# Optimization experiments

Measured on AMD Instinct MI355X. Metric: run time of the kernel, lower is better.

The kernel has to match this reference:

```python
import jax, jax.numpy as jnp
import numpy as np

N_INST = 131072      # total patches across all bags
D_EMB = 512          # VGG16 pooling='max' output dim
ATT_UNITS = 128
CLS_UNITS = 512
NUM_BAGS = 256


def setup_inputs() -> dict:
    key = jax.random.key(0)
    ks = jax.random.split(key, 16)
    first_emb = jax.random.normal(ks[0], (N_INST, D_EMB), dtype=jnp.float32)
    first_lab = jnp.sort(jax.random.randint(ks[1], (N_INST,), 0, NUM_BAGS)).astype(jnp.int64)
    s = 0.02
    return {
        "first_emb": first_emb,
        "first_lab": first_lab,
        # first-level attention head: Dense(tanh) -> Dense(1, sigmoid)
        "W_a1": jax.random.normal(ks[2], (D_EMB, ATT_UNITS), dtype=jnp.float32) * s,
        "b_a1": jnp.zeros((ATT_UNITS,), dtype=jnp.float32),
        "w_o1": jax.random.normal(ks[3], (ATT_UNITS, 1), dtype=jnp.float32) * s,
        "b_o1": jnp.zeros((1,), dtype=jnp.float32),
        # second-level attention head
        "W_a2": jax.random.normal(ks[4], (D_EMB, ATT_UNITS), dtype=jnp.float32) * s,
        "b_a2": jnp.zeros((ATT_UNITS,), dtype=jnp.float32),
        "w_o2": jax.random.normal(ks[5], (ATT_UNITS, 1), dtype=jnp.float32) * s,
        "b_o2": jnp.zeros((1,), dtype=jnp.float32),
        # classifier: Dense(CLS_UNITS, linear) -> Dense(1, sigmoid)
        "W_c": jax.random.normal(ks[6], (D_EMB, CLS_UNITS), dtype=jnp.float32) * s,
        "b_c": jnp.zeros((CLS_UNITS,), dtype=jnp.float32),
        "w_out": jax.random.normal(ks[7], (CLS_UNITS, 1), dtype=jnp.float32) * s,
        "b_out": jnp.zeros((1,), dtype=jnp.float32),
    }


def reference(first_emb, first_lab, W_a1, b_a1, w_o1, b_o1,
              W_a2, b_a2, w_o2, b_o2, W_c, b_c, w_out, b_out):
    # --- first-level (instance) attention ---
    a1 = jnp.tanh(first_emb @ W_a1 + b_a1)                 # [N, A]
    att1 = jax.nn.sigmoid(a1 @ w_o1 + b_o1)                # [N, 1]
    # tf: transpose(softmax(transpose(att))) == softmax over the N axis (global)
    fst_att = jax.nn.softmax(att1, axis=0)                 # [N, 1]
    # --- per-bag attention-weighted sum (fused segment reduce) ---
    # replaces the python loop of gather_nd + matmul over contiguous bags
    second_emb = jax.ops.segment_sum(fst_att * first_emb, first_lab,
                                     num_segments=NUM_BAGS)  # [B, D]
    # --- second-level (bag) attention ---
    a2 = jnp.tanh(second_emb @ W_a2 + b_a2)                # [B, A]
    att2 = jax.nn.sigmoid(a2 @ w_o2 + b_o2)                # [B, 1]
    snd_att = jax.nn.softmax(att2.T, axis=-1)              # [1, B]
    outer_bag_emb = snd_att @ second_emb                   # [1, D]
    # --- classifier (dropout is identity at inference) ---
    h = outer_bag_emb @ W_c + b_c                          # [1, CLS]
    pred = jax.nn.sigmoid(h @ w_out + b_out)               # [1, 1]
    return pred
```

## Files before the change

### kernel.cpp

```cpp
#include <hip/hip_runtime.h>
#include <cstdint>
#include <cstddef>

#define N_INST 131072
#define D_EMB  512
#define ATT    128
#define NBAGS  256
#define TILE_I 32
#define LDA    520
#define NBLK   512
#define NTILES (N_INST / TILE_I)
#define TPB    (NTILES / NBLK)

typedef __attribute__((ext_vector_type(8))) short  bf16x8;
typedef __attribute__((ext_vector_type(4))) float  f32x4;
typedef __attribute__((ext_vector_type(4))) unsigned short u16x4;


__device__ inline unsigned short f2b(float f) {
    unsigned u = __builtin_bit_cast(unsigned, f);
    u += 0x7FFFu + ((u >> 16) & 1u);
    return (unsigned short)(u >> 16);
}

__device__ inline float fast_tanh(float x) {
    float e = __expf(2.f * x);
    return 1.f - 2.f / (e + 1.f);
}

__global__ __launch_bounds__(256) void k_prep_wt(
    const float* __restrict__ Wa1, unsigned short* __restrict__ Wt)
{
    const int n = blockIdx.x;
    for (int k = threadIdx.x; k < D_EMB; k += 256)
        Wt[(size_t)n * D_EMB + k] = f2b(Wa1[(size_t)k * ATT + n]);
}

__global__ __launch_bounds__(256, 2) void k_att1(
    const float* __restrict__ emb, const int* __restrict__ lab,
    const unsigned short* __restrict__ Wt, const float* __restrict__ ba1,
    const float* __restrict__ wo1, const float* __restrict__ bo1,
    float* __restrict__ rawr, int R, float* __restrict__ Z1)
{
    __shared__ unsigned short Ash[2][TILE_I * LDA];
    __shared__ float att4[4][TILE_I];
    __shared__ float sval[TILE_I];
    __shared__ int   labs[2][TILE_I];

    const int t  = threadIdx.x;
    const int w  = t >> 6;
    const int l  = t & 63;
    const int l4 = l & 15;
    const int h4 = l >> 4;
    const int n0 = 16 * (2 * w) + l4;
    const int n1 = 16 * (2 * w + 1) + l4;
    float* __restrict__ raw = rawr + (size_t)(blockIdx.x % R) * (NBAGS * D_EMB);

    const float ba1v0 = ba1[n0], ba1v1 = ba1[n1];
    const float wo1v0 = wo1[n0], wo1v1 = wo1[n1];
    float z1acc = 0.f;

    {
        const size_t i0 = (size_t)blockIdx.x * TILE_I;
        float4 v[16];
        #pragma unroll
        for (int j = 0; j < 16; ++j) {
            int idx = j * 256 + t;
            int row = idx >> 7;
            int c4  = (idx & 127) * 4;
            v[j] = *reinterpret_cast<const float4*>(&emb[(i0 + row) * D_EMB + c4]);
        }
        if (t < TILE_I) labs[0][t] = lab[i0 + t];
        #pragma unroll
        for (int j = 0; j < 16; ++j) {
            int idx = j * 256 + t;
            int row = idx >> 7;
            int c4  = (idx & 127) * 4;
            u16x4 b = { f2b(v[j].x), f2b(v[j].y), f2b(v[j].z), f2b(v[j].w) };
            *reinterpret_cast<u16x4*>(&Ash[0][row * LDA + c4]) = b;
        }
    }
    __syncthreads();

    int p = 0;
    for (int it = 0; it < TPB; ++it) {
        const bool hasNext = (it + 1 < TPB);
        const size_t i0n = ((size_t)blockIdx.x + (size_t)(it + 1) * NBLK) * TILE_I;

        float4 v[16];
        int nlab = 0;
        if (hasNext) {
            #pragma unroll
            for (int j = 0; j < 16; ++j) {
                int idx = j * 256 + t;
                int row = idx >> 7;
                int c4  = (idx & 127) * 4;
                v[j] = *reinterpret_cast<const float4*>(
                    &emb[(i0n + row) * D_EMB + c4]);
            }
            if (t < TILE_I) nlab = lab[i0n + t];
        }

        f32x4 acc00 = {0.f,0.f,0.f,0.f}, acc01 = {0.f,0.f,0.f,0.f};
        f32x4 acc10 = {0.f,0.f,0.f,0.f}, acc11 = {0.f,0.f,0.f,0.f};
        #pragma unroll
        for (int ks = 0; ks < 16; ++ks) {
            bf16x8 b0 = *reinterpret_cast<const bf16x8*>(
                &Wt[(size_t)n0 * D_EMB + 32 * ks + 8 * h4]);
            bf16x8 b1 = *reinterpret_cast<const bf16x8*>(
                &Wt[(size_t)n1 * D_EMB + 32 * ks + 8 * h4]);
            bf16x8 a0 = *reinterpret_cast<const bf16x8*>(
                &Ash[p][(l4) * LDA + 32 * ks + 8 * h4]);
            bf16x8 a1 = *reinterpret_cast<const bf16x8*>(
                &Ash[p][(16 + l4) * LDA + 32 * ks + 8 * h4]);
            acc00 = __builtin_amdgcn_mfma_f32_16x16x32_bf16(a0, b0, acc00, 0, 0, 0);
            acc01 = __builtin_amdgcn_mfma_f32_16x16x32_bf16(a0, b1, acc01, 0, 0, 0);
            acc10 = __builtin_amdgcn_mfma_f32_16x16x32_bf16(a1, b0, acc10, 0, 0, 0);
            acc11 = __builtin_amdgcn_mfma_f32_16x16x32_bf16(a1, b1, acc11, 0, 0, 0);
        }

        #pragma unroll
        for (int rt = 0; rt < 2; ++rt) {
            #pragma unroll
            for (int reg = 0; reg < 4; ++reg) {
                float pp = fast_tanh((rt ? acc10[reg] : acc00[reg]) + ba1v0) * wo1v0
                         + fast_tanh((rt ? acc11[reg] : acc01[reg]) + ba1v1) * wo1v1;
                pp += __shfl_xor(pp, 1);
                pp += __shfl_xor(pp, 2);
                pp += __shfl_xor(pp, 4);
                pp += __shfl_xor(pp, 8);
                if (l4 == 0) att4[w][16 * rt + 4 * h4 + reg] = pp;
            }
        }
        __syncthreads();
        if (t < TILE_I) {
            float a  = att4[0][t] + att4[1][t] + att4[2][t] + att4[3][t] + bo1[0];
            float sg = 1.f / (1.f + __expf(-a));
            sval[t]  = __expf(sg);
        }
        __syncthreads();
        if (t < TILE_I) {
            float z = sval[t];
            z += __shfl_xor(z, 1);
            z += __shfl_xor(z, 2);
            z += __shfl_xor(z, 4);
            z += __shfl_xor(z, 8);
            z += __shfl_xor(z, 16);
            if (t == 0) z1acc += z;
        }

        int s0 = 0;
        while (s0 < TILE_I) {
            int bag = labs[p][s0];
            int s1 = s0 + 1;
            while (s1 < TILE_I && labs[p][s1] == bag) ++s1;
            float a0 = 0.f, a1 = 0.f;
            for (int ii = s0; ii < s1; ++ii) {
                unsigned u = *reinterpret_cast<const unsigned*>(
                    &Ash[p][(size_t)ii * LDA + 2 * t]);
                float lo = __builtin_bit_cast(float, u << 16);
                float hi = __builtin_bit_cast(float, u & 0xffff0000u);
                float s  = sval[ii];
                a0 = fmaf(s, lo, a0);
                a1 = fmaf(s, hi, a1);
            }
            atomicAdd(&raw[bag * D_EMB + 2 * t], a0);
            atomicAdd(&raw[bag * D_EMB + 2 * t + 1], a1);
            s0 = s1;
        }
        __syncthreads();

        if (hasNext) {
            #pragma unroll
            for (int j = 0; j < 16; ++j) {
                int idx = j * 256 + t;
                int row = idx >> 7;
                int c4  = (idx & 127) * 4;
                u16x4 b = { f2b(v[j].x), f2b(v[j].y), f2b(v[j].z), f2b(v[j].w) };
                *reinterpret_cast<u16x4*>(&Ash[p ^ 1][row * LDA + c4]) = b;
            }
            if (t < TILE_I) labs[p ^ 1][t] = nlab;
        }
        __syncthreads();
        p ^= 1;
    }
    if (t == 0) atomicAdd(Z1, z1acc);
}

__global__ __launch_bounds__(128) void k_att2(
    const float* __restrict__ Wa2, const float* __restrict__ ba2,
    const float* __restrict__ wo2, const float* __restrict__ bo2,
    float* __restrict__ rawr, int R, const float* __restrict__ Z1,
    float* __restrict__ e2, float* __restrict__ Z2)
{
    __shared__ float sec[D_EMB];
    __shared__ float hh[2];
    const int b = blockIdx.x;
    const int t = threadIdx.x;
    const float zinv = 1.f / Z1[0];
    for (int d = t; d < D_EMB; d += 128) {
        float s = 0.f;
        for (int r = 0; r < R; ++r)
            s += rawr[(size_t)r * (NBAGS * D_EMB) + b * D_EMB + d];
        float v = s * zinv;
        rawr[b * D_EMB + d] = v;
        sec[d] = v;
    }
    __syncthreads();
    float dot = 0.f;
    #pragma unroll 8
    for (int d = 0; d < D_EMB; ++d) dot = fmaf(sec[d], Wa2[d * ATT + t], dot);
    float h = fast_tanh(dot + ba2[t]) * wo2[t];
    #pragma unroll
    for (int m = 1; m < 64; m <<= 1) h += __shfl_xor(h, m);
    if ((t & 63) == 0) hh[t >> 6] = h;
    __syncthreads();
    if (t == 0) {
        float a  = hh[0] + hh[1] + bo2[0];
        float sg = 1.f / (1.f + __expf(-a));
        float e  = __expf(sg);
        e2[b] = e;
        atomicAdd(Z2, e);
    }
}

__global__ __launch_bounds__(256) void k_v(
    const float* __restrict__ Wc, const float* __restrict__ wout,
    float* __restrict__ v)
{
    const int t   = threadIdx.x;
    const int row = blockIdx.x * 8 + (t >> 5);
    const int l   = t & 31;
    float s = 0.f;
    #pragma unroll 4
    for (int c = l; c < 512; c += 32) s = fmaf(Wc[(size_t)row * 512 + c], wout[c], s);
    #pragma unroll
    for (int m = 1; m < 32; m <<= 1) s += __shfl_xor(s, m);
    if (l == 0) v[row] = s;
}

__global__ __launch_bounds__(256) void k_pool(
    const float* __restrict__ raw, const float* __restrict__ e2,
    float* __restrict__ outer)
{
    const int t  = threadIdx.x;
    const int b0 = blockIdx.x * 32;
    float o0 = 0.f, o1 = 0.f;
    for (int b = b0; b < b0 + 32; ++b) {
        float wgt = e2[b];
        float2 r = *reinterpret_cast<const float2*>(&raw[b * D_EMB + 2 * t]);
        o0 = fmaf(wgt, r.x, o0);
        o1 = fmaf(wgt, r.y, o1);
    }
    atomicAdd(&outer[2 * t], o0);
    atomicAdd(&outer[2 * t + 1], o1);
}

__global__ __launch_bounds__(256) void k_cls(
    const float* __restrict__ outer, const float* __restrict__ Z2,
    const float* __restrict__ v, const float* __restrict__ bc,
    const float* __restrict__ wout, const float* __restrict__ bout,
    float* __restrict__ out)
{
    __shared__ float pp[4];
    const int t = threadIdx.x;
    const float z2inv = 1.f / Z2[0];
    float p = (outer[2 * t] * v[2 * t] + outer[2 * t + 1] * v[2 * t + 1]) * z2inv
            + bc[2 * t] * wout[2 * t] + bc[2 * t + 1] * wout[2 * t + 1];
    #pragma unroll
    for (int m = 1; m < 64; m <<= 1) p += __shfl_xor(p, m);
    if ((t & 63) == 0) pp[t >> 6] = p;
    __syncthreads();
    if (t == 0) {
        float s = pp[0] + pp[1] + pp[2] + pp[3] + bout[0];
        out[0] = 1.f / (1.f + __expf(-s));
    }
}

extern "C" void kernel_launch(void* const* d_in, const int* in_sizes, int n_in,
                              void* d_out, int out_size, void* d_ws, size_t ws_size,
                              hipStream_t stream)
{
    const float* emb  = (const float*)d_in[0];
    const int*   lab  = (const int*)d_in[1];
    const float* Wa1  = (const float*)d_in[2];
    const float* ba1  = (const float*)d_in[3];
    const float* wo1  = (const float*)d_in[4];
    const float* bo1  = (const float*)d_in[5];
    const float* Wa2  = (const float*)d_in[6];
    const float* ba2  = (const float*)d_in[7];
    const float* wo2  = (const float*)d_in[8];
    const float* bo2  = (const float*)d_in[9];
    const float* Wc   = (const float*)d_in[10];
    const float* bc   = (const float*)d_in[11];
    const float* wout = (const float*)d_in[12];
    const float* bout = (const float*)d_in[13];

    float* ws    = (float*)d_ws;
    float* Z1    = ws + 0;
    float* Z2    = ws + 1;
    float* v     = ws + 16;
    float* e2    = ws + 1024;
    float* outer = ws + 1536;
    unsigned short* Wt = (unsigned short*)(ws + 4096);
    float* rawr  = ws + 36864;

    const size_t need8 = ((size_t)36864 + 8u * NBAGS * D_EMB) * sizeof(float);
    const int R = (ws_size >= need8) ? 8 : 1;

    hipMemsetAsync(d_ws, 0, ((size_t)36864 + (size_t)R * NBAGS * D_EMB) * sizeof(float), stream);

    hipLaunchKernelGGL(k_prep_wt, dim3(ATT),   dim3(256), 0, stream, Wa1, Wt);
    hipLaunchKernelGGL(k_v,       dim3(64),    dim3(256), 0, stream, Wc, wout, v);
    hipLaunchKernelGGL(k_att1,    dim3(NBLK),  dim3(256), 0, stream,
                       emb, lab, Wt, ba1, wo1, bo1, rawr, R, Z1);
    hipLaunchKernelGGL(k_att2,    dim3(NBAGS), dim3(128), 0, stream,
                       Wa2, ba2, wo2, bo2, rawr, R, Z1, e2, Z2);
    hipLaunchKernelGGL(k_pool,    dim3(8),     dim3(256), 0, stream,
                       rawr, e2, outer);
    hipLaunchKernelGGL(k_cls,     dim3(1),     dim3(256), 0, stream,
                       outer, Z2, v, bc, wout, bout, (float*)d_out);
}
```

Measured before the change: 136.0 us.

## Use 512-thread blocks with contiguous tiles, register-resident weights, and run-carried bag sums

Switches the attention kernel to 256 blocks of 512 threads (8 waves, one 16-column slice each), so each wave holds its Wa1 bf16 fragments in registers instead of reloading them from global memory on every tile. Each block now walks a contiguous range of tiles instead of a strided one. Because labels are sorted, each thread can carry a running per-bag sum across tiles and issue one atomic per bag change rather than per tile segment. Two barriers are merged and replaced by a lighter lgkmcnt-wait barrier macro. In exchange the launch has half as many blocks at one block per CU, and register pressure rises.

```diff
diff --git a/kernel.cpp b/kernel.cpp
--- a/kernel.cpp
+++ b/kernel.cpp
@@ -8,13 +8,19 @@
 #define NBAGS  256
 #define TILE_I 32
 #define LDA    520
-#define NBLK   512
+#define NBLK   256
 #define NTILES (N_INST / TILE_I)
 #define TPB    (NTILES / NBLK)
 
 typedef __attribute__((ext_vector_type(8))) short  bf16x8;
 typedef __attribute__((ext_vector_type(4))) float  f32x4;
 typedef __attribute__((ext_vector_type(4))) unsigned short u16x4;
+
+#define BAR() do {                                             \
+    asm volatile("s_waitcnt lgkmcnt(0)" ::: "memory");          \
+    __builtin_amdgcn_s_barrier();                               \
+    asm volatile("" ::: "memory");                              \
+} while (0)
 
 
 __device__ inline unsigned short f2b(float f) {
@@ -36,14 +42,14 @@
         Wt[(size_t)n * D_EMB + k] = f2b(Wa1[(size_t)k * ATT + n]);
 }
 
-__global__ __launch_bounds__(256, 2) void k_att1(
+__global__ __launch_bounds__(512, 1) void k_att1(
     const float* __restrict__ emb, const int* __restrict__ lab,
     const unsigned short* __restrict__ Wt, const float* __restrict__ ba1,
     const float* __restrict__ wo1, const float* __restrict__ bo1,
     float* __restrict__ rawr, int R, float* __restrict__ Z1)
 {
     __shared__ unsigned short Ash[2][TILE_I * LDA];
-    __shared__ float att4[4][TILE_I];
+    __shared__ float att8[8][TILE_I];
     __shared__ float sval[TILE_I];
     __shared__ int   labs[2][TILE_I];
 
@@ -52,47 +58,56 @@
     const int l  = t & 63;
     const int l4 = l & 15;
     const int h4 = l >> 4;
-    const int n0 = 16 * (2 * w) + l4;
-    const int n1 = 16 * (2 * w + 1) + l4;
+    const int n0 = 16 * w + l4;
+    const size_t tile0 = (size_t)blockIdx.x * TPB;
     float* __restrict__ raw = rawr + (size_t)(blockIdx.x % R) * (NBAGS * D_EMB);
 
-    const float ba1v0 = ba1[n0], ba1v1 = ba1[n1];
-    const float wo1v0 = wo1[n0], wo1v1 = wo1[n1];
-    float z1acc = 0.f;
+    const float ba1v = ba1[n0];
+    const float wo1v = wo1[n0];
+
+    bf16x8 bfrag[16];
+    #pragma unroll
+    for (int ks = 0; ks < 16; ++ks)
+        bfrag[ks] = *reinterpret_cast<const bf16x8*>(
+            &Wt[(size_t)n0 * D_EMB + 32 * ks + 8 * h4]);
 
     {
-        const size_t i0 = (size_t)blockIdx.x * TILE_I;
-        float4 v[16];
+        const size_t i0 = tile0 * TILE_I;
+        float4 v[8];
         #pragma unroll
-        for (int j = 0; j < 16; ++j) {
-            int idx = j * 256 + t;
+        for (int j = 0; j < 8; ++j) {
+            int idx = j * 512 + t;
             int row = idx >> 7;
             int c4  = (idx & 127) * 4;
             v[j] = *reinterpret_cast<const float4*>(&emb[(i0 + row) * D_EMB + c4]);
         }
         if (t < TILE_I) labs[0][t] = lab[i0 + t];
         #pragma unroll
-        for (int j = 0; j < 16; ++j) {
-            int idx = j * 256 + t;
+        for (int j = 0; j < 8; ++j) {
+            int idx = j * 512 + t;
             int row = idx >> 7;
             int c4  = (idx & 127) * 4;
             u16x4 b = { f2b(v[j].x), f2b(v[j].y), f2b(v[j].z), f2b(v[j].w) };
             *reinterpret_cast<u16x4*>(&Ash[0][row * LDA + c4]) = b;
         }
     }
-    __syncthreads();
-
-    int p = 0;
+    BAR();
+
+    int   cur_bag = -1;
+    float a_run   = 0.f;
+    float z1acc   = 0.f;
+    int   p       = 0;
+
     for (int it = 0; it < TPB; ++it) {
         const bool hasNext = (it + 1 < TPB);
-        const size_t i0n = ((size_t)blockIdx.x + (size_t)(it + 1) * NBLK) * TILE_I;
-
-        float4 v[16];
+        const size_t i0n = (tile0 + it + 1) * TILE_I;
+
+        float4 v[8];
         int nlab = 0;
         if (hasNext) {
             #pragma unroll
-            for (int j = 0; j < 16; ++j) {
-                int idx = j * 256 + t;
+            for (int j = 0; j < 8; ++j) {
+                int idx = j * 512 + t;
                 int row = idx >> 7;
                 int c4  = (idx & 127) * 4;
                 v[j] = *reinterpret_cast<const float4*>(
@@ -101,46 +116,38 @@
             if (t < TILE_I) nlab = lab[i0n + t];
         }
 
-        f32x4 acc00 = {0.f,0.f,0.f,0.f}, acc01 = {0.f,0.f,0.f,0.f};
-        f32x4 acc10 = {0.f,0.f,0.f,0.f}, acc11 = {0.f,0.f,0.f,0.f};
+        f32x4 acc0 = {0.f,0.f,0.f,0.f}, acc1 = {0.f,0.f,0.f,0.f};
         #pragma unroll
         for (int ks = 0; ks < 16; ++ks) {
-            bf16x8 b0 = *reinterpret_cast<const bf16x8*>(
-                &Wt[(size_t)n0 * D_EMB + 32 * ks + 8 * h4]);
-            bf16x8 b1 = *reinterpret_cast<const bf16x8*>(
-                &Wt[(size_t)n1 * D_EMB + 32 * ks + 8 * h4]);
             bf16x8 a0 = *reinterpret_cast<const bf16x8*>(
                 &Ash[p][(l4) * LDA + 32 * ks + 8 * h4]);
             bf16x8 a1 = *reinterpret_cast<const bf16x8*>(
                 &Ash[p][(16 + l4) * LDA + 32 * ks + 8 * h4]);
-            acc00 = __builtin_amdgcn_mfma_f32_16x16x32_bf16(a0, b0, acc00, 0, 0, 0);
-            acc01 = __builtin_amdgcn_mfma_f32_16x16x32_bf16(a0, b1, acc01, 0, 0, 0);
-            acc10 = __builtin_amdgcn_mfma_f32_16x16x32_bf16(a1, b0, acc10, 0, 0, 0);
-            acc11 = __builtin_amdgcn_mfma_f32_16x16x32_bf16(a1, b1, acc11, 0, 0, 0);
+            acc0 = __builtin_amdgcn_mfma_f32_16x16x32_bf16(a0, bfrag[ks], acc0, 0, 0, 0);
+            acc1 = __builtin_amdgcn_mfma_f32_16x16x32_bf16(a1, bfrag[ks], acc1, 0, 0, 0);
         }
 
         #pragma unroll
         for (int rt = 0; rt < 2; ++rt) {
             #pragma unroll
             for (int reg = 0; reg < 4; ++reg) {
-                float pp = fast_tanh((rt ? acc10[reg] : acc00[reg]) + ba1v0) * wo1v0
-                         + fast_tanh((rt ? acc11[reg] : acc01[reg]) + ba1v1) * wo1v1;
+                float pp = fast_tanh((rt ? acc1[reg] : acc0[reg]) + ba1v) * wo1v;
                 pp += __shfl_xor(pp, 1);
                 pp += __shfl_xor(pp, 2);
                 pp += __shfl_xor(pp, 4);
                 pp += __shfl_xor(pp, 8);
-                if (l4 == 0) att4[w][16 * rt + 4 * h4 + reg] = pp;
+                if (l4 == 0) att8[w][16 * rt + 4 * h4 + reg] = pp;
             }
         }
-        __syncthreads();
+        BAR();
         if (t < TILE_I) {
-            float a  = att4[0][t] + att4[1][t] + att4[2][t] + att4[3][t] + bo1[0];
+            float a = bo1[0];
+            #pragma unroll
+            for (int ww = 0; ww < 8; ++ww) a += att8[ww][t];
             float sg = 1.f / (1.f + __expf(-a));
-            sval[t]  = __expf(sg);
-        }
-        __syncthreads();
-        if (t < TILE_I) {
-            float z = sval[t];
+            float s  = __expf(sg);
+            sval[t]  = s;
+            float z = s;
             z += __shfl_xor(z, 1);
             z += __shfl_xor(z, 2);
             z += __shfl_xor(z, 4);
@@ -148,32 +155,35 @@
             z += __shfl_xor(z, 16);
             if (t == 0) z1acc += z;
         }
-
-        int s0 = 0;
-        while (s0 < TILE_I) {
-            int bag = labs[p][s0];
-            int s1 = s0 + 1;
-            while (s1 < TILE_I && labs[p][s1] == bag) ++s1;
-            float a0 = 0.f, a1 = 0.f;
-            for (int ii = s0; ii < s1; ++ii) {
-                unsigned u = *reinterpret_cast<const unsigned*>(
-                    &Ash[p][(size_t)ii * LDA + 2 * t]);
-                float lo = __builtin_bit_cast(float, u << 16);
-                float hi = __builtin_bit_cast(float, u & 0xffff0000u);
-                float s  = sval[ii];
-                a0 = fmaf(s, lo, a0);
-                a1 = fmaf(s, hi, a1);
+        BAR();
+
+        {
+            int s0 = 0;
+            while (s0 < TILE_I) {
+                int bag = labs[p][s0];
+                int s1 = s0 + 1;
+                while (s1 < TILE_I && labs[p][s1] == bag) ++s1;
+                if (bag != cur_bag) {
+                    if (cur_bag >= 0)
+                        atomicAdd(&raw[cur_bag * D_EMB + t], a_run);
+                    a_run = 0.f;
+                    cur_bag = bag;
+                }
+                #pragma unroll 8
+                for (int ii = s0; ii < s1; ++ii) {
+                    unsigned short us = Ash[p][(size_t)ii * LDA + t];
+                    float e = __builtin_bit_cast(float, (unsigned)us << 16);
+                    a_run = fmaf(sval[ii], e, a_run);
+                }
+                s0 = s1;
             }
-            atomicAdd(&raw[bag * D_EMB + 2 * t], a0);
-            atomicAdd(&raw[bag * D_EMB + 2 * t + 1], a1);
-            s0 = s1;
-        }
-        __syncthreads();
+        }
+        BAR();
 
         if (hasNext) {
             #pragma unroll
-            for (int j = 0; j < 16; ++j) {
-                int idx = j * 256 + t;
+            for (int j = 0; j < 8; ++j) {
+                int idx = j * 512 + t;
                 int row = idx >> 7;
                 int c4  = (idx & 127) * 4;
                 u16x4 b = { f2b(v[j].x), f2b(v[j].y), f2b(v[j].z), f2b(v[j].w) };
@@ -181,9 +191,11 @@
             }
             if (t < TILE_I) labs[p ^ 1][t] = nlab;
         }
-        __syncthreads();
+        BAR();
         p ^= 1;
     }
+
+    if (cur_bag >= 0) atomicAdd(&raw[cur_bag * D_EMB + t], a_run);
     if (t == 0) atomicAdd(Z1, z1acc);
 }
 
@@ -312,7 +324,7 @@
 
     hipLaunchKernelGGL(k_prep_wt, dim3(ATT),   dim3(256), 0, stream, Wa1, Wt);
     hipLaunchKernelGGL(k_v,       dim3(64),    dim3(256), 0, stream, Wc, wout, v);
-    hipLaunchKernelGGL(k_att1,    dim3(NBLK),  dim3(256), 0, stream,
+    hipLaunchKernelGGL(k_att1,    dim3(NBLK),  dim3(512), 0, stream,
                        emb, lab, Wt, ba1, wo1, bo1, rawr, R, Z1);
     hipLaunchKernelGGL(k_att2,    dim3(NBAGS), dim3(128), 0, stream,
                        Wa2, ba2, wo2, bo2, rawr, R, Z1, e2, Z2);
```

Result: slower. 152.2 us (+11.9%).

## Give blocks contiguous tiles and carry per-bag sums in registers across tiles

Applied to the files above, without the earlier changes.

Each block now processes a contiguous run of tiles instead of tiles strided across the grid, so consecutive tiles mostly share a bag. The per-thread bag accumulator is kept in registers across tiles and flushed with atomics only when the bag changes, which cuts global atomic traffic. The weighted sum now reads fp32 embeddings straight from global memory, where they are likely still in cache, instead of the bf16 copy in shared memory, which improves accuracy. One block barrier is also folded away. The cost is a second global read of every tile, which may miss cache and add memory traffic.

```diff
diff --git a/kernel.cpp b/kernel.cpp
--- a/kernel.cpp
+++ b/kernel.cpp
@@ -54,14 +54,14 @@
     const int h4 = l >> 4;
     const int n0 = 16 * (2 * w) + l4;
     const int n1 = 16 * (2 * w + 1) + l4;
+    const size_t tile0 = (size_t)blockIdx.x * TPB;
     float* __restrict__ raw = rawr + (size_t)(blockIdx.x % R) * (NBAGS * D_EMB);
 
     const float ba1v0 = ba1[n0], ba1v1 = ba1[n1];
     const float wo1v0 = wo1[n0], wo1v1 = wo1[n1];
-    float z1acc = 0.f;
 
     {
-        const size_t i0 = (size_t)blockIdx.x * TILE_I;
+        const size_t i0 = tile0 * TILE_I;
         float4 v[16];
         #pragma unroll
         for (int j = 0; j < 16; ++j) {
@@ -82,10 +82,15 @@
     }
     __syncthreads();
 
-    int p = 0;
+    int   cur_bag = -1;
+    float ar0 = 0.f, ar1 = 0.f;
+    float z1acc = 0.f;
+    int   p = 0;
+
     for (int it = 0; it < TPB; ++it) {
         const bool hasNext = (it + 1 < TPB);
-        const size_t i0n = ((size_t)blockIdx.x + (size_t)(it + 1) * NBLK) * TILE_I;
+        const size_t i0  = (tile0 + it) * TILE_I;
+        const size_t i0n = (tile0 + it + 1) * TILE_I;
 
         float4 v[16];
         int nlab = 0;
@@ -132,43 +137,6 @@
                 if (l4 == 0) att4[w][16 * rt + 4 * h4 + reg] = pp;
             }
         }
-        __syncthreads();
-        if (t < TILE_I) {
-            float a  = att4[0][t] + att4[1][t] + att4[2][t] + att4[3][t] + bo1[0];
-            float sg = 1.f / (1.f + __expf(-a));
-            sval[t]  = __expf(sg);
-        }
-        __syncthreads();
-        if (t < TILE_I) {
-            float z = sval[t];
-            z += __shfl_xor(z, 1);
-            z += __shfl_xor(z, 2);
-            z += __shfl_xor(z, 4);
-            z += __shfl_xor(z, 8);
-            z += __shfl_xor(z, 16);
-            if (t == 0) z1acc += z;
-        }
-
-        int s0 = 0;
-        while (s0 < TILE_I) {
-            int bag = labs[p][s0];
-            int s1 = s0 + 1;
-            while (s1 < TILE_I && labs[p][s1] == bag) ++s1;
-            float a0 = 0.f, a1 = 0.f;
-            for (int ii = s0; ii < s1; ++ii) {
-                unsigned u = *reinterpret_cast<const unsigned*>(
-                    &Ash[p][(size_t)ii * LDA + 2 * t]);
-                float lo = __builtin_bit_cast(float, u << 16);
-                float hi = __builtin_bit_cast(float, u & 0xffff0000u);
-                float s  = sval[ii];
-                a0 = fmaf(s, lo, a0);
-                a1 = fmaf(s, hi, a1);
-            }
-            atomicAdd(&raw[bag * D_EMB + 2 * t], a0);
-            atomicAdd(&raw[bag * D_EMB + 2 * t + 1], a1);
-            s0 = s1;
-        }
-        __syncthreads();
 
         if (hasNext) {
             #pragma unroll
@@ -179,10 +147,57 @@
                 u16x4 b = { f2b(v[j].x), f2b(v[j].y), f2b(v[j].z), f2b(v[j].w) };
                 *reinterpret_cast<u16x4*>(&Ash[p ^ 1][row * LDA + c4]) = b;
             }
-            if (t < TILE_I) labs[p ^ 1][t] = nlab;
         }
         __syncthreads();
+
+        if (t < TILE_I) {
+            float a  = att4[0][t] + att4[1][t] + att4[2][t] + att4[3][t] + bo1[0];
+            float sg = 1.f / (1.f + __expf(-a));
+            float s  = __expf(sg);
+            sval[t]  = s;
+            if (hasNext) labs[p ^ 1][t] = nlab;
+            float z = s;
+            z += __shfl_xor(z, 1);
+            z += __shfl_xor(z, 2);
+            z += __shfl_xor(z, 4);
+            z += __shfl_xor(z, 8);
+            z += __shfl_xor(z, 16);
+            if (t == 0) z1acc += z;
+        }
+        __syncthreads();
+
+        {
+            int s0 = 0;
+            while (s0 < TILE_I) {
+                int bag = labs[p][s0];
+                int s1 = s0 + 1;
+                while (s1 < TILE_I && labs[p][s1] == bag) ++s1;
+                if (bag != cur_bag) {
+                    if (cur_bag >= 0) {
+                        atomicAdd(&raw[cur_bag * D_EMB + 2 * t], ar0);
+                        atomicAdd(&raw[cur_bag * D_EMB + 2 * t + 1], ar1);
+                    }
+                    ar0 = 0.f; ar1 = 0.f; cur_bag = bag;
+                }
+                const float* ebase = emb + (i0 + s0) * D_EMB + 2 * t;
+                int len = s1 - s0;
+                #pragma unroll 8
+                for (int ii = 0; ii < len; ++ii) {
+                    float2 e = *reinterpret_cast<const float2*>(
+                        ebase + (size_t)ii * D_EMB);
+                    float s = sval[s0 + ii];
+                    ar0 = fmaf(s, e.x, ar0);
+                    ar1 = fmaf(s, e.y, ar1);
+                }
+                s0 = s1;
+            }
+        }
         p ^= 1;
+    }
+
+    if (cur_bag >= 0) {
+        atomicAdd(&raw[cur_bag * D_EMB + 2 * t], ar0);
+        atomicAdd(&raw[cur_bag * D_EMB + 2 * t + 1], ar1);
     }
     if (t == 0) atomicAdd(Z1, z1acc);
 }
```

Result: slower. 199.8 us (+47.0%).
